# Kernel optimization log

Hardware: AMD Instinct MI355X
Metric: run time of the kernel (lower is better)

The kernel has to match this reference:

```python
import jax, jax.numpy as jnp
import numpy as np

BETA = 0.25
TEMPERATURE = 0.1
PROB_EMA_DECAY = 0.9
EPS_NORM = 1e-12  # torch F.normalize eps
EPS_LOG = 1e-8


def _l2_normalize(x):
    n = jnp.linalg.norm(x, axis=-1, keepdims=True)
    return x / jnp.maximum(n, EPS_NORM)


def setup_inputs() -> dict:
    key = jax.random.key(0)
    k1, k2 = jax.random.split(key)
    B, T, D, K = 8, 2048, 128, 8192
    z = jax.random.normal(k1, (B, T, D), dtype=jnp.float32)
    # nn.Embedding init: uniform(-1/D, 1/D)
    codebook = jax.random.uniform(k2, (K, D), dtype=jnp.float32,
                                  minval=-1.0 / D, maxval=1.0 / D)
    probs_ema = jnp.full((K,), 1.0 / K, dtype=jnp.float32)
    return {"z": z, "codebook": codebook, "probs_ema": probs_ema}


def reference(z, codebook, probs_ema):
    K, D = codebook.shape
    orig_shape = z.shape
    zf = z.reshape(-1, D)                      # [N, D]
    N = zf.shape[0]

    z_norm = _l2_normalize(zf)                 # [N, D]
    emb_norm = _l2_normalize(codebook)         # [K, D]
    cos_sim = jnp.einsum('nd,kd->nk', z_norm, emb_norm)  # [N, K]

    idx = jnp.argmax(cos_sim, axis=1)          # [N] int
    z_q = codebook[idx].reshape(orig_shape)

    counts = jnp.bincount(idx, length=K)
    e_mean = counts.astype(jnp.float32) / N
    perplexity = jnp.exp(-jnp.sum(e_mean * jnp.log(e_mean + EPS_LOG)))

    sg = jax.lax.stop_gradient
    commit_loss = jnp.mean((sg(z_q) - z) ** 2) + BETA * jnp.mean((z_q - sg(z)) ** 2)
    z_q_ste = z + sg(z_q - z)

    log_probs = jax.nn.log_softmax(cos_sim / TEMPERATURE, axis=1)  # [N, K]
    P_avg = jnp.mean(jnp.exp(log_probs), axis=0) + EPS_LOG         # [K]
    entropy_loss = -jnp.sum(P_avg * jnp.log(P_avg))

    # --- no-grad EMA bookkeeping + dead-code reactivation (state update) ---
    ema = sg(PROB_EMA_DECAY * probs_ema + (1.0 - PROB_EMA_DECAY) * e_mean)
    threshold = 0.0125 / K
    dead = ema < threshold                     # [K] bool
    rank = jnp.cumsum(dead.astype(jnp.int32)) - 1  # rank among dead codes
    sel = dead & (rank < N)                    # only first min(num_dead, N) dead codes
    perm = jax.random.permutation(jax.random.key(1), N)
    src = perm[jnp.clip(rank, 0, N - 1)]       # [K] source token indices
    new_codebook = jnp.where(sel[:, None], sg(zf)[src], codebook)  # updated state
    ema = jnp.where(sel, 1.0 / K, ema)
    del new_codebook  # stateful side-effect in torch; not part of forward output

    return (z_q_ste, commit_loss, perplexity, entropy_loss, jnp.min(ema))
```

## Files before the change

### kernel.cpp

```cpp
#include <hip/hip_runtime.h>

constexpr int NTOK = 16384;
constexpr int KCB  = 8192;
constexpr int DDIM = 128;
constexpr int OUT_MAIN = NTOK * DDIM;

typedef _Float16 f16x8 __attribute__((ext_vector_type(8)));
typedef _Float16 f16x2 __attribute__((ext_vector_type(2)));
typedef float    f32x4 __attribute__((ext_vector_type(4)));

constexpr float S12 = 0.0035222047f;
constexpr float A12   = 29546.39f;
constexpr float SCHRB = 1064866805.0f;
constexpr float RTHR_RAW = 4.096f;

__device__ __forceinline__ float fexp2raw(float raw) {
  return __int_as_float((int)fmaf(raw, A12, SCHRB));
}

__global__ __launch_bounds__(256) void norm_k(const float* __restrict__ z,
                                              const float* __restrict__ cb,
                                              _Float16* __restrict__ znh,
                                              _Float16* __restrict__ enh,
                                              float* __restrict__ zin,
                                              float* __restrict__ ein) {
  int lane = threadIdx.x & 63;
  int w    = threadIdx.x >> 6;
  int row  = blockIdx.x * 4 + w;
  const float* src;
  _Float16* dh;
  float* nv;
  if (row < NTOK) {
    src = z + (size_t)row * DDIM;
    dh = znh + (size_t)row * DDIM;
    nv = zin + row;
  } else {
    int r = row - NTOK;
    src = cb + (size_t)r * DDIM;
    dh = enh + (size_t)r * DDIM;
    nv = ein + r;
  }
  float2 v = reinterpret_cast<const float2*>(src)[lane];
  float ss = v.x * v.x + v.y * v.y;
#pragma unroll
  for (int m = 1; m < 64; m <<= 1) ss += __shfl_xor(ss, m);
  float rn = 1.0f / fmaxf(sqrtf(ss), 1e-12f);
  if (lane == 0) *nv = rn;
  float rs = rn * 64.0f;
  f16x2 h2;
  h2.x = (_Float16)(v.x * rs);
  h2.y = (_Float16)(v.y * rs);
  reinterpret_cast<f16x2*>(dh)[lane] = h2;
}

__global__ __launch_bounds__(256) void transp_k(const float* __restrict__ cb,
                                                float* __restrict__ cbT) {
  __shared__ float t[32][65];
  int tid = threadIdx.x;
  int k0 = blockIdx.x * 64, d0 = blockIdx.y * 32;
#pragma unroll
  for (int p = 0; p < 8; ++p) {
    int idx = p * 256 + tid;
    int r = idx >> 5, c = idx & 31;
    t[c][r] = cb[(size_t)(k0 + r) * DDIM + d0 + c];
  }
  __syncthreads();
#pragma unroll
  for (int p = 0; p < 8; ++p) {
    int idx = p * 256 + tid;
    int c = idx >> 6, r = idx & 63;
    cbT[(size_t)(d0 + c) * KCB + k0 + r] = t[c][r];
  }
}

__global__ __launch_bounds__(256, 3) void pass1m(const _Float16* __restrict__ znh,
                                                 const _Float16* __restrict__ enh,
                                                 float* __restrict__ pb1,
                                                 int* __restrict__ pidx,
                                                 float* __restrict__ pb2,
                                                 float* __restrict__ pL) {
  __shared__ float4 mbuf[32][4][16];
  int tid = threadIdx.x, w = tid >> 6, l = tid & 63;
  int q = l >> 4, lr = l & 15;
  int part = blockIdx.x;
  int c0 = part * 256 + w * 64;
  int r0 = blockIdx.y * 512;

  f16x8 bh[4][4];
#pragma unroll
  for (int tt = 0; tt < 4; ++tt)
#pragma unroll
    for (int dc = 0; dc < 4; ++dc) {
      int col = c0 + tt * 16 + lr;
      bh[tt][dc] = *reinterpret_cast<const f16x8*>(enh + (size_t)col * DDIM + dc * 32 + q * 8);
    }

  const char* zp = reinterpret_cast<const char*>(
      znh + (size_t)(r0 + lr) * DDIM + q * 8);
  f16x8 zc[4];
#pragma unroll
  for (int dc = 0; dc < 4; ++dc)
    zc[dc] = *reinterpret_cast<const f16x8*>(zp + dc * 64);
  zp += 4096;

  for (int rt = 0; rt < 32; ++rt) {
    f16x8 zn[4];
#pragma unroll
    for (int dc = 0; dc < 4; ++dc)
      zn[dc] = *reinterpret_cast<const f16x8*>(zp + dc * 64);
    zp += 4096;

    f32x4 hh[4];
#pragma unroll
    for (int tt = 0; tt < 4; ++tt)
#pragma unroll
      for (int e = 0; e < 4; ++e) hh[tt][e] = 0.0f;
#pragma unroll
    for (int dc = 0; dc < 4; ++dc)
#pragma unroll
      for (int tt = 0; tt < 4; ++tt)
        hh[tt] = __builtin_amdgcn_mfma_f32_16x16x32_f16(bh[tt][dc], zc[dc], hh[tt], 0, 0, 0);

    float s[16];
#pragma unroll
    for (int tt = 0; tt < 4; ++tt)
#pragma unroll
      for (int rg = 0; rg < 4; ++rg)
        s[tt * 4 + rg] = hh[tt][rg];

    float g1[4], g2[4];
    int   gi[4];
#pragma unroll
    for (int g = 0; g < 4; ++g) {
      float a = s[g * 4];
      float b = -3e38f;
      int   ix = 0;
#pragma unroll
      for (int j = 1; j < 4; ++j) {
        float sv = s[g * 4 + j];
        b = fmaxf(b, fminf(sv, a));
        ix = (sv > a) ? j : ix;
        a = fmaxf(a, sv);
      }
      g1[g] = a; g2[g] = b; gi[g] = g * 4 + ix;
    }
    float h1a = fmaxf(g1[0], g1[1]);
    int   hia = (g1[1] > g1[0]) ? gi[1] : gi[0];
    float h2a = fmaxf(fminf(g1[0], g1[1]), fmaxf(g2[0], g2[1]));
    float h1b = fmaxf(g1[2], g1[3]);
    int   hib = (g1[3] > g1[2]) ? gi[3] : gi[2];
    float h2b = fmaxf(fminf(g1[2], g1[3]), fmaxf(g2[2], g2[3]));
    float m1 = fmaxf(h1a, h1b);
    int   ii = (h1b > h1a) ? hib : hia;
    float m2 = fmaxf(fminf(h1a, h1b), fmaxf(h2a, h2b));
    int kk = c0 + q * 4 + ((ii >> 2) << 4) + (ii & 3);

    float ex[16];
#pragma unroll
    for (int i = 0; i < 16; ++i) ex[i] = fexp2raw(s[i]);
#pragma unroll
    for (int st = 1; st < 16; st <<= 1)
#pragma unroll
      for (int i = 0; i < 16; i += 2 * st) ex[i] += ex[i + st];
    float Lr = ex[0];

#pragma unroll
    for (int m = 16; m <= 32; m <<= 1) {
      float o1 = __shfl_xor(m1, m), o2 = __shfl_xor(m2, m), oL = __shfl_xor(Lr, m);
      int ok = __shfl_xor(kk, m);
      Lr += oL;
      m2 = fmaxf(fminf(m1, o1), fmaxf(m2, o2));
      if (o1 > m1 || (o1 == m1 && ok < kk)) kk = ok;
      m1 = fmaxf(m1, o1);
    }
    if (l < 16) mbuf[rt][w][l] = make_float4(m1, __int_as_float(kk), m2, Lr);

#pragma unroll
    for (int dc = 0; dc < 4; ++dc) zc[dc] = zn[dc];
  }

  __syncthreads();
  int base = part * NTOK + r0;
  for (int e = tid; e < 512; e += 256) {
    int rt = e >> 4, rr = e & 15;
    float4 a = mbuf[rt][0][rr];
    float B1 = a.x, B2 = a.z, LL = a.w;
    int BI = __float_as_int(a.y);
#pragma unroll
    for (int ww = 1; ww < 4; ++ww) {
      float4 o = mbuf[rt][ww][rr];
      LL += o.w;
      B2 = fmaxf(fminf(B1, o.x), fmaxf(B2, o.z));
      if (o.x > B1) BI = __float_as_int(o.y);
      B1 = fmaxf(B1, o.x);
    }
    int n = base + rt * 16 + rr;
    pb1[n] = B1; pidx[n] = BI; pb2[n] = B2; pL[n] = LL;
  }
}

__global__ __launch_bounds__(256) void merge2_k(const float* __restrict__ pb1,
                                                const int* __restrict__ pidx,
                                                const float* __restrict__ pb2,
                                                const float* __restrict__ pL,
                                                float* __restrict__ lse,
                                                int* __restrict__ idxb,
                                                int* __restrict__ counts,
                                                int* __restrict__ rcount,
                                                int* __restrict__ rlist) {
  int n = blockIdx.x * 256 + threadIdx.x;
  float B1 = pb1[n], B2 = pb2[n], LL = pL[n];
  int BI = pidx[n];
  for (int p = 1; p < 32; ++p) {
    int off = p * NTOK + n;
    float ob1 = pb1[off], ob2 = pb2[off], oL = pL[off];
    int oi = pidx[off];
    LL += oL;
    B2 = fmaxf(fminf(B1, ob1), fmaxf(B2, ob2));
    if (ob1 > B1) BI = oi;
    B1 = fmaxf(B1, ob1);
  }
  lse[n] = __log2f(LL);
  idxb[n] = BI;
  atomicAdd(&counts[BI], 1);
  if (B1 - B2 < RTHR_RAW) {
    int s = atomicAdd(rcount, 1);
    rlist[s] = n;
  }
}

__global__ __launch_bounds__(256) void rescue2a_k(const float* __restrict__ z,
                                                  const float* __restrict__ cbT,
                                                  const float* __restrict__ zin,
                                                  const float* __restrict__ ein,
                                                  const int* __restrict__ rcount,
                                                  const int* __restrict__ rlist,
                                                  float* __restrict__ rbufv,
                                                  int* __restrict__ rbufi) {
  __shared__ float zr[8][DDIM];
  __shared__ float wbv[4][8];
  __shared__ int   wbi[4][8];
  int tid = threadIdx.x;
  int ch  = blockIdx.y;
  int cnt = *rcount;
  int ngrp = (cnt + 7) >> 3;
  for (int g = blockIdx.x; g < ngrp; g += gridDim.x) {
    int base = g * 8;
    int rows = min(8, cnt - base);
    __syncthreads();
    int rr0 = tid >> 5, d4 = tid & 31;
    if (rr0 < rows) {
      int n = rlist[base + rr0];
      float rnz = zin[n];
      float4 v = reinterpret_cast<const float4*>(z + (size_t)n * DDIM)[d4];
      v.x *= rnz; v.y *= rnz; v.z *= rnz; v.w *= rnz;
      reinterpret_cast<float4*>(zr[rr0])[d4] = v;
    }
    __syncthreads();
    int c0 = ch * 1024 + tid * 4;
    float4 acc[8];
#pragma unroll
    for (int r = 0; r < 8; ++r) acc[r] = make_float4(0.f, 0.f, 0.f, 0.f);
#pragma unroll 2
    for (int d = 0; d < DDIM; ++d) {
      float4 e = reinterpret_cast<const float4*>(cbT + (size_t)d * KCB)[ch * 256 + tid];
#pragma unroll
      for (int r = 0; r < 8; ++r) {
        float zd = zr[r][d];
        acc[r].x = fmaf(e.x, zd, acc[r].x);
        acc[r].y = fmaf(e.y, zd, acc[r].y);
        acc[r].z = fmaf(e.z, zd, acc[r].z);
        acc[r].w = fmaf(e.w, zd, acc[r].w);
      }
    }
    float4 ev = reinterpret_cast<const float4*>(ein)[ch * 256 + tid];
    float bv[8];
    int   bi[8];
#pragma unroll
    for (int r = 0; r < 8; ++r) {
      float s0 = acc[r].x * ev.x, s1 = acc[r].y * ev.y;
      float s2 = acc[r].z * ev.z, s3 = acc[r].w * ev.w;
      float B = s0; int I = c0;
      if (s1 > B) { B = s1; I = c0 + 1; }
      if (s2 > B) { B = s2; I = c0 + 2; }
      if (s3 > B) { B = s3; I = c0 + 3; }
      bv[r] = B; bi[r] = I;
    }
#pragma unroll
    for (int m = 1; m < 64; m <<= 1) {
#pragma unroll
      for (int r = 0; r < 8; ++r) {
        float ov = __shfl_xor(bv[r], m);
        int   oi = __shfl_xor(bi[r], m);
        if (ov > bv[r] || (ov == bv[r] && oi < bi[r])) { bv[r] = ov; bi[r] = oi; }
      }
    }
    int wv = tid >> 6;
    if ((tid & 63) == 0) {
#pragma unroll
      for (int r = 0; r < 8; ++r) { wbv[wv][r] = bv[r]; wbi[wv][r] = bi[r]; }
    }
    __syncthreads();
    if (tid < rows) {
      int r = tid;
      float BV = wbv[0][r];
      int   BI = wbi[0][r];
#pragma unroll
      for (int ww = 1; ww < 4; ++ww)
        if (wbv[ww][r] > BV || (wbv[ww][r] == BV && wbi[ww][r] < BI)) {
          BV = wbv[ww][r]; BI = wbi[ww][r];
        }
      rbufv[(base + r) * 8 + ch] = BV;
      rbufi[(base + r) * 8 + ch] = BI;
    }
  }
}

__global__ __launch_bounds__(256) void rescue2b_k(const int* __restrict__ rcount,
                                                  const int* __restrict__ rlist,
                                                  const float* __restrict__ rbufv,
                                                  const int* __restrict__ rbufi,
                                                  int* __restrict__ idxb,
                                                  int* __restrict__ counts) {
  int cnt = *rcount;
  for (int ri = blockIdx.x * 256 + threadIdx.x; ri < cnt; ri += gridDim.x * 256) {
    float BV = rbufv[ri * 8];
    int   BI = rbufi[ri * 8];
#pragma unroll
    for (int ch = 1; ch < 8; ++ch) {
      float v = rbufv[ri * 8 + ch];
      int   i = rbufi[ri * 8 + ch];
      if (v > BV) { BV = v; BI = i; }
    }
    int n = rlist[ri];
    int old = idxb[n];
    if (BI != old) {
      atomicSub(&counts[old], 1);
      atomicAdd(&counts[BI], 1);
      idxb[n] = BI;
    }
  }
}

__global__ __launch_bounds__(256) void rescue_k(const float* __restrict__ z,
                                                const float* __restrict__ cb,
                                                const float* __restrict__ zin,
                                                const float* __restrict__ ein,
                                                const int* __restrict__ rcount,
                                                const int* __restrict__ rlist,
                                                int* __restrict__ idxb,
                                                int* __restrict__ counts) {
  __shared__ float rbv[4];
  __shared__ int   rbi[4];
  int tid = threadIdx.x, wv = tid >> 6, l = tid & 63;
  int half = l >> 5, ld = l & 31;
  int cnt = *rcount;
  for (int ri = blockIdx.x; ri < cnt; ri += gridDim.x) {
    int n = rlist[ri];
    __syncthreads();
    float rnz = zin[n];
    float4 zv = reinterpret_cast<const float4*>(z + (size_t)n * DDIM)[ld];
    zv.x *= rnz; zv.y *= rnz; zv.z *= rnz; zv.w *= rnz;
    float bv = -3e38f;
    int   bi = 0;
    for (int c0 = wv * 2; c0 < KCB; c0 += 8) {
      int c = c0 + half;
      float4 ev = reinterpret_cast<const float4*>(cb + (size_t)c * DDIM)[ld];
      float p = zv.x * ev.x;
      p = fmaf(zv.y, ev.y, p);
      p = fmaf(zv.z, ev.z, p);
      p = fmaf(zv.w, ev.w, p);
#pragma unroll
      for (int m = 1; m < 32; m <<= 1) p += __shfl_xor(p, m);
      float s = p * ein[c];
      if (s > bv) { bv = s; bi = c; }
    }
#pragma unroll
    for (int m = 1; m < 64; m <<= 1) {
      float ov = __shfl_xor(bv, m);
      int   oi = __shfl_xor(bi, m);
      if (ov > bv || (ov == bv && oi < bi)) { bv = ov; bi = oi; }
    }
    if (l == 0) { rbv[wv] = bv; rbi[wv] = bi; }
    __syncthreads();
    if (tid == 0) {
#pragma unroll
      for (int ww = 1; ww < 4; ++ww)
        if (rbv[ww] > bv || (rbv[ww] == bv && rbi[ww] < bi)) { bv = rbv[ww]; bi = rbi[ww]; }
      int old = idxb[n];
      if (bi != old) {
        atomicSub(&counts[old], 1);
        atomicAdd(&counts[bi], 1);
        idxb[n] = bi;
      }
    }
  }
}

__global__ __launch_bounds__(256, 4) void pass2r(const _Float16* __restrict__ znh,
                                                 const _Float16* __restrict__ enh,
                                                 const float* __restrict__ lse,
                                                 float* __restrict__ Ppart) {
  int tid = threadIdx.x, w = tid >> 6, l = tid & 63;
  int q = l >> 4, lr = l & 15;
  int part = blockIdx.x;
  int c0 = part * 256 + w * 64;
  int r0 = blockIdx.y * 512;

  f16x8 bh[4][4];
#pragma unroll
  for (int tt = 0; tt < 4; ++tt)
#pragma unroll
    for (int dc = 0; dc < 4; ++dc) {
      int col = c0 + tt * 16 + lr;
      bh[tt][dc] = *reinterpret_cast<const f16x8*>(enh + (size_t)col * DDIM + dc * 32 + q * 8);
    }

  f32x4 psum[4];
#pragma unroll
  for (int tt = 0; tt < 4; ++tt)
#pragma unroll
    for (int e = 0; e < 4; ++e) psum[tt][e] = 0.0f;

  const char* zp = reinterpret_cast<const char*>(
      znh + (size_t)(r0 + lr) * DDIM + q * 8);
  const float* lp = lse + r0 + lr;

  for (int rt = 0; rt < 32; ++rt) {
    f16x8 zh[4];
#pragma unroll
    for (int dc = 0; dc < 4; ++dc)
      zh[dc] = *reinterpret_cast<const f16x8*>(zp + dc * 64);
    zp += 4096;
    float lsez = lp[rt * 16];
    float bias = fmaf(lsez, -8388608.0f, SCHRB);
    f32x4 hh[4];
#pragma unroll
    for (int tt = 0; tt < 4; ++tt)
#pragma unroll
      for (int e = 0; e < 4; ++e) hh[tt][e] = 0.0f;
#pragma unroll
    for (int dc = 0; dc < 4; ++dc)
#pragma unroll
      for (int tt = 0; tt < 4; ++tt)
        hh[tt] = __builtin_amdgcn_mfma_f32_16x16x32_f16(bh[tt][dc], zh[dc], hh[tt], 0, 0, 0);
#pragma unroll
    for (int tt = 0; tt < 4; ++tt)
#pragma unroll
      for (int rg = 0; rg < 4; ++rg)
        psum[tt][rg] += __int_as_float((int)fmaf(hh[tt][rg], A12, bias));
  }

#pragma unroll
  for (int m = 1; m < 16; m <<= 1)
#pragma unroll
    for (int tt = 0; tt < 4; ++tt)
#pragma unroll
      for (int rg = 0; rg < 4; ++rg)
        psum[tt][rg] += __shfl_xor(psum[tt][rg], m);

  if (lr == 0) {
    float* dst = Ppart + (size_t)blockIdx.y * KCB + c0;
#pragma unroll
    for (int tt = 0; tt < 4; ++tt)
#pragma unroll
      for (int rg = 0; rg < 4; ++rg)
        dst[tt * 16 + q * 4 + rg] = psum[tt][rg];
  }
}

__global__ __launch_bounds__(256) void k3(const float* __restrict__ z,
                                          const float* __restrict__ cb,
                                          const int* __restrict__ idxb,
                                          float* __restrict__ out,
                                          float* __restrict__ cpart) {
  int tid = threadIdx.x;
  int e   = blockIdx.x * 256 + tid;
  int n   = e >> 5;
  int q   = e & 31;
  int id  = idxb[n];
  float4 c4 = reinterpret_cast<const float4*>(cb)[id * 32 + q];
  float4 z4 = reinterpret_cast<const float4*>(z)[e];
  float4 o;
  o.x = z4.x + (c4.x - z4.x);
  o.y = z4.y + (c4.y - z4.y);
  o.z = z4.z + (c4.z - z4.z);
  o.w = z4.w + (c4.w - z4.w);
  reinterpret_cast<float4*>(out)[e] = o;
  float dx = c4.x - z4.x, dy = c4.y - z4.y, dz = c4.z - z4.z, dw = c4.w - z4.w;
  float ds = dx * dx + dy * dy + dz * dz + dw * dw;
#pragma unroll
  for (int m = 1; m < 64; m <<= 1) ds += __shfl_xor(ds, m);
  __shared__ float wsum[4];
  if ((tid & 63) == 0) wsum[tid >> 6] = ds;
  __syncthreads();
  if (tid == 0) cpart[blockIdx.x] = wsum[0] + wsum[1] + wsum[2] + wsum[3];
}

__global__ __launch_bounds__(256) void reduceP(const float* __restrict__ Ppart,
                                               float* __restrict__ Psum,
                                               int rows) {
  int k = blockIdx.x * 256 + threadIdx.x;
  float s = 0.0f;
  for (int b = 0; b < rows; ++b) s += Ppart[(size_t)b * KCB + k];
  Psum[k] = s;
}

__global__ __launch_bounds__(256) void finalk(const int* __restrict__ counts,
                                              const float* __restrict__ Psum,
                                              const float* __restrict__ pema,
                                              const float* __restrict__ cpart,
                                              float* __restrict__ out) {
  int tid = threadIdx.x;
  float s1 = 0.0f, s2 = 0.0f, cs = 0.0f, mn = 1e30f;
  const float invN = 1.0f / (float)NTOK;
  const float thr  = 0.0125f / (float)KCB;
  const float invK = 1.0f / (float)KCB;
  for (int k = tid; k < KCB; k += 256) {
    float e = (float)counts[k] * invN;
    s1 += e * logf(e + 1e-8f);
    float pa = Psum[k] * invN + 1e-8f;
    s2 += pa * logf(pa);
    float ema  = 0.9f * pema[k] + 0.1f * e;
    float emaf = (ema < thr) ? invK : ema;
    mn = fminf(mn, emaf);
  }
  for (int b = tid; b < 2048; b += 256) cs += cpart[b];
#pragma unroll
  for (int m = 1; m < 64; m <<= 1) {
    s1 += __shfl_xor(s1, m);
    s2 += __shfl_xor(s2, m);
    cs += __shfl_xor(cs, m);
    mn = fminf(mn, __shfl_xor(mn, m));
  }
  __shared__ float r1[4], r2[4], r3[4], r4[4];
  if ((tid & 63) == 0) {
    int w = tid >> 6;
    r1[w] = s1; r2[w] = s2; r3[w] = cs; r4[w] = mn;
  }
  __syncthreads();
  if (tid == 0) {
    float S1 = r1[0] + r1[1] + r1[2] + r1[3];
    float S2 = r2[0] + r2[1] + r2[2] + r2[3];
    float CS = r3[0] + r3[1] + r3[2] + r3[3];
    float MN = fminf(fminf(r4[0], r4[1]), fminf(r4[2], r4[3]));
    out[OUT_MAIN + 0] = 1.25f * CS / (float)OUT_MAIN;
    out[OUT_MAIN + 1] = expf(-S1);
    out[OUT_MAIN + 2] = -S2;
    out[OUT_MAIN + 3] = MN;
  }
}

extern "C" void kernel_launch(void* const* d_in, const int* in_sizes, int n_in,
                              void* d_out, int out_size, void* d_ws, size_t ws_size,
                              hipStream_t stream) {
  const float* z    = (const float*)d_in[0];
  const float* cb   = (const float*)d_in[1];
  const float* pema = (const float*)d_in[2];
  float* out = (float*)d_out;
  char*  ws  = (char*)d_ws;

  _Float16* znh = (_Float16*)(ws + 0x000000);
  _Float16* enh = (_Float16*)(ws + 0x800000);
  char* sb = ws + 0xC00000;
  float* zin    = (float*)(sb + 0x00000);
  float* ein    = (float*)(sb + 0x10000);
  float* lse    = (float*)(sb + 0x18000);
  int*   idxb   = (int*)  (sb + 0x28000);
  int*   counts = (int*)  (sb + 0x38000);
  int*   rcount = (int*)  (sb + 0x40000);
  int*   rlist  = (int*)  (sb + 0x41000);
  float* Psum   = (float*)(sb + 0x51000);
  float* cpart  = (float*)(sb + 0x59000);
  char* pb = ws + 0xD00000;
  float* pb1  = (float*)(pb + 0x000000);
  int*   pidx = (int*)  (pb + 0x200000);
  float* pb2  = (float*)(pb + 0x400000);
  float* pL   = (float*)(pb + 0x600000);
  float* rbufv = (float*)(pb + 0x000000);
  int*   rbufi = (int*)  (pb + 0x100000);
  float* Ppart = (float*)(ws + 0x400000);
  float* cbT   = (float*)(ws + 0x1500000);

  bool havecbt = ws_size >= (size_t)0x1900000;

  hipMemsetAsync(counts, 0, KCB * sizeof(int) + 0x400, stream);

  norm_k <<<(NTOK + KCB) / 4, 256, 0, stream>>>(z, cb, znh, enh, zin, ein);
  if (havecbt)
    transp_k<<<dim3(KCB / 64, DDIM / 32), 256, 0, stream>>>(cb, cbT);
  pass1m <<<dim3(32, 32),     256, 0, stream>>>(znh, enh, pb1, pidx, pb2, pL);
  merge2_k<<<NTOK / 256,      256, 0, stream>>>(pb1, pidx, pb2, pL, lse, idxb, counts, rcount, rlist);
  if (havecbt) {
    rescue2a_k<<<dim3(256, 8), 256, 0, stream>>>(z, cbT, zin, ein, rcount, rlist, rbufv, rbufi);
    rescue2b_k<<<64,           256, 0, stream>>>(rcount, rlist, rbufv, rbufi, idxb, counts);
  } else {
    rescue_k<<<1024,           256, 0, stream>>>(z, cb, zin, ein, rcount, rlist, idxb, counts);
  }
  pass2r <<<dim3(32, 32),     256, 0, stream>>>(znh, enh, lse, Ppart);
  k3     <<<NTOK * DDIM / 4 / 256, 256, 0, stream>>>(z, cb, idxb, out, cpart);
  reduceP<<<KCB / 256,        256, 0, stream>>>(Ppart, Psum, 32);
  finalk <<<1,                256, 0, stream>>>(counts, Psum, pema, cpart, out);
}
```

Measured before the change: 237.8 us.

## Software-pipeline MFMA and epilogue with double-buffered accumulators in argmax kernel

Restructures the row-tile loop so the MFMA for the next tile is issued before the argmax/softmax epilogue of the current tile, using two accumulator sets and two z register buffers. The goal is to overlap matrix-core latency with the VALU-heavy epilogue and shuffles, instead of stalling on MFMA results each iteration. The cost is extra VGPR pressure from the doubled accumulators and buffers, which could lower occupancy or cause spills. The final iteration also issues one load past the last tile.

```diff
diff --git a/kernel.cpp b/kernel.cpp
--- a/kernel.cpp
+++ b/kernel.cpp
@@ -97,20 +97,14 @@
 
   const char* zp = reinterpret_cast<const char*>(
       znh + (size_t)(r0 + lr) * DDIM + q * 8);
-  f16x8 zc[4];
-#pragma unroll
-  for (int dc = 0; dc < 4; ++dc)
-    zc[dc] = *reinterpret_cast<const f16x8*>(zp + dc * 64);
-  zp += 4096;
-
-  for (int rt = 0; rt < 32; ++rt) {
-    f16x8 zn[4];
+
+  auto loadz = [&](f16x8 (&zz)[4]) {
 #pragma unroll
     for (int dc = 0; dc < 4; ++dc)
-      zn[dc] = *reinterpret_cast<const f16x8*>(zp + dc * 64);
+      zz[dc] = *reinterpret_cast<const f16x8*>(zp + dc * 64);
     zp += 4096;
-
-    f32x4 hh[4];
+  };
+  auto domfma = [&](f32x4 (&hh)[4], const f16x8 (&zz)[4]) {
 #pragma unroll
     for (int tt = 0; tt < 4; ++tt)
 #pragma unroll
@@ -119,8 +113,9 @@
     for (int dc = 0; dc < 4; ++dc)
 #pragma unroll
       for (int tt = 0; tt < 4; ++tt)
-        hh[tt] = __builtin_amdgcn_mfma_f32_16x16x32_f16(bh[tt][dc], zc[dc], hh[tt], 0, 0, 0);
-
+        hh[tt] = __builtin_amdgcn_mfma_f32_16x16x32_f16(bh[tt][dc], zz[dc], hh[tt], 0, 0, 0);
+  };
+  auto epilogue = [&](const f32x4 (&hh)[4], int rt) {
     float s[16];
 #pragma unroll
     for (int tt = 0; tt < 4; ++tt)
@@ -174,9 +169,21 @@
       m1 = fmaxf(m1, o1);
     }
     if (l < 16) mbuf[rt][w][l] = make_float4(m1, __int_as_float(kk), m2, Lr);
-
-#pragma unroll
-    for (int dc = 0; dc < 4; ++dc) zc[dc] = zn[dc];
+  };
+
+  f16x8 zA[4], zB[4];
+  f32x4 hhA[4], hhB[4];
+  loadz(zA);
+  domfma(hhA, zA);
+  loadz(zB);
+#pragma unroll 1
+  for (int it = 0; it < 16; ++it) {
+    loadz(zA);
+    domfma(hhB, zB);
+    epilogue(hhA, 2 * it);
+    loadz(zB);
+    if (it < 15) domfma(hhA, zA);
+    epilogue(hhB, 2 * it + 1);
   }
 
   __syncthreads();
```

After: 243.5 us. +2.4%, slower.
